# Kernel tuning notes

Hardware: AMD Instinct MI355X
Metric: run time of the kernel (lower is better)

## Reference

```python
import jax, jax.numpy as jnp
import numpy as np

EMB = 256
N_NODES = 100000
N_EDGES = 500000
N_REL = 10
REL_DIM = 64
HID = 128
HEADS = 4
HEAD_DIM = HID // HEADS


def setup_inputs() -> dict:
    key = jax.random.key(0)
    ks = jax.random.split(key, 16)
    s = lambda i, shape: jax.random.normal(ks[i], shape, dtype=jnp.float32) * 0.05
    return {
        "node_embeddings": jax.random.normal(ks[0], (N_NODES, EMB), dtype=jnp.float32),
        "edge_index": jax.random.randint(ks[1], (2, N_EDGES), 0, N_NODES),
        "relation_type": jax.random.randint(ks[2], (N_EDGES,), 0, N_REL),
        "rel_emb": s(3, (N_REL, REL_DIM)),
        "W_edge": s(4, (2 * EMB, HID)), "b_edge": jnp.zeros((HID,), jnp.float32),
        "W_q": s(5, (REL_DIM, HID)), "b_q": jnp.zeros((HID,), jnp.float32),
        "W_k": s(6, (HID, HID)), "b_k": jnp.zeros((HID,), jnp.float32),
        "W_v": s(7, (HID, HID)), "b_v": jnp.zeros((HID,), jnp.float32),
        "W_o1": s(8, (HID, HID)), "b_o1": jnp.zeros((HID,), jnp.float32),
        "W_o2": s(9, (HID, 1)), "b_o2": jnp.zeros((1,), jnp.float32),
    }


def reference(node_embeddings, edge_index, relation_type, rel_emb,
              W_edge, b_edge, W_q, b_q, W_k, b_k, W_v, b_v,
              W_o1, b_o1, W_o2, b_o2):
    # Gather endpoint features: [E, 2*EMB]
    src = node_embeddings[edge_index[0]]
    tgt = node_embeddings[edge_index[1]]
    edge_features = jnp.concatenate([src, tgt], axis=1)
    # Edge MLP (dropout is identity at eval): [E, HID]
    edge_hidden = jax.nn.relu(edge_features @ W_edge + b_edge)
    # Relation embedding lookup: [E, REL_DIM]
    rel = rel_emb[relation_type]
    E = edge_hidden.shape[0]
    Q = (rel @ W_q + b_q).reshape(E, HEADS, HEAD_DIM)
    K = (edge_hidden @ W_k + b_k).reshape(E, HEADS, HEAD_DIM)
    V = (edge_hidden @ W_v + b_v).reshape(E, HEADS, HEAD_DIM)
    scale = jnp.sqrt(jnp.float32(HEAD_DIM))
    scores = jnp.sum(Q * K, axis=-1) / scale          # [E, HEADS]
    attn = jax.nn.softmax(scores, axis=-1)            # softmax over heads
    attended = (attn[..., None] * V).reshape(E, HID)
    output = attended + edge_hidden
    # Output MLP: Linear->ReLU->Linear(1)
    h = jax.nn.relu(output @ W_o1 + b_o1)
    score = (h @ W_o2 + b_o2).squeeze(-1)             # [E]
    return score
```

## Files before the change

### kernel.cpp

```cpp
#include <hip/hip_runtime.h>

#define EMB   256
#define HID   128
#define RELD  64
#define NREL  10
#define TE    128

typedef __attribute__((ext_vector_type(8)))  short bf16x8;
typedef __attribute__((ext_vector_type(16))) float f32x16;

__device__ __forceinline__ float bf16_to_f32(unsigned short u) {
    union { unsigned int i; float f; } v;
    v.i = ((unsigned int)u) << 16;
    return v.f;
}

__device__ __forceinline__ unsigned short f32_to_bf16(float x) {
    union { unsigned int i; float f; } v;
    v.f = x;
    unsigned int b = v.i;
    unsigned int rounded = b + 0x7fffu + ((b >> 16) & 1u);
    return (unsigned short)(rounded >> 16);
}

template <bool F32>
__device__ __forceinline__ float ldx(const void* p, size_t i) {
    if (F32) return ((const float*)p)[i];
    return bf16_to_f32(((const unsigned short*)p)[i]);
}

__device__ __forceinline__ bool detect_f32(const void* nodeEmb) {
    const float* f = (const float*)nodeEmb;
    float x = f[(threadIdx.x & 63) * 997];
    bool sane = isfinite(x) && fabsf(x) < 1.0e6f;
    unsigned long long m = __ballot(sane);
    return __popcll(m) >= 48;
}

__device__ __forceinline__ void gload16(const void* g, void* l) {
    __builtin_amdgcn_global_load_lds(
        (const __attribute__((address_space(1))) unsigned int*)g,
        (__attribute__((address_space(3))) unsigned int*)l, 16, 0, 0);
}

#define WAITVL(n) asm volatile("s_waitcnt vmcnt(" #n ") lgkmcnt(0)" ::: "memory")

__device__ __forceinline__ void sbar() {
    __builtin_amdgcn_sched_barrier(0);
    __builtin_amdgcn_s_barrier();
    __builtin_amdgcn_sched_barrier(0);
}
__device__ __forceinline__ void bar_lds() {
    asm volatile("s_waitcnt lgkmcnt(0)" ::: "memory");
    sbar();
}

template <bool F32>
__device__ void prep_body(int vb, const void* W_edge, const void* W_k,
                          const void* W_v, const void* W_o1, const void* rel_emb,
                          const void* W_q, const void* b_q,
                          unsigned short* WTe, unsigned short* WTk,
                          unsigned short* WTv, unsigned short* WTo1, float* Qtab)
{
    if (vb < 448) {
        int idx = vb * 256 + threadIdx.x;
        if (idx < 65536) {
            int kc = idx >> 12, e = idx & 4095;
            int g = e >> 3, j = e & 7;
            int col = g & 127, kg = g >> 7;
            int k = kc * 32 + kg * 8 + j;
            WTe[idx] = f32_to_bf16(ldx<F32>(W_edge, (size_t)k * HID + col));
        } else if (idx < 65536 + 16384) {
            int i = idx - 65536;
            int kc = i >> 12, e = i & 4095;
            int g = e >> 3, j = e & 7;
            int col = g & 127, kg = (g >> 7) & 3;
            int k = kc * 32 + kg * 8 + j;
            WTk[i] = f32_to_bf16(ldx<F32>(W_k, (size_t)k * HID + col));
        } else if (idx < 65536 + 2 * 16384) {
            int i = idx - 65536 - 16384;
            int kc = i >> 12, e = i & 4095;
            int g = e >> 3, j = e & 7;
            int col = g & 127, kg = (g >> 7) & 3;
            int k = kc * 32 + kg * 8 + j;
            WTv[i] = f32_to_bf16(ldx<F32>(W_v, (size_t)k * HID + col));
        } else {
            int i = idx - 65536 - 2 * 16384;
            int kc = i >> 12, e = i & 4095;
            int g = e >> 3, j = e & 7;
            int col = g & 127, kg = (g >> 7) & 3;
            int k = kc * 32 + kg * 8 + j;
            WTo1[i] = f32_to_bf16(ldx<F32>(W_o1, (size_t)k * HID + col));
        }
    } else {
        const int t = threadIdx.x;
        const int c = t & (HID - 1);
        const int h = t >> 7;
        for (int r = h; r < NREL; r += 2) {
            float acc = 0.f;
            for (int d = 0; d < RELD; ++d)
                acc += ldx<F32>(rel_emb, r * RELD + d) * ldx<F32>(W_q, (size_t)d * HID + c);
            Qtab[r * HID + c] = acc + ldx<F32>(b_q, c);
        }
    }
}

__global__ void prep_kernel(const void* nodeEmb,
                            const void* W_edge, const void* W_k, const void* W_v,
                            const void* W_o1, const void* rel_emb, const void* W_q,
                            const void* b_q,
                            unsigned short* WTe, unsigned short* WTk,
                            unsigned short* WTv, unsigned short* WTo1, float* Qtab,
                            unsigned short* nodeBf16, int convBlocks,
                            unsigned long long nodeElems)
{
    bool f32 = detect_f32(nodeEmb);
    int b = blockIdx.x;
    if (b < convBlocks) {
        if (!f32) return;
        unsigned long long i = (unsigned long long)b * 2048ull + threadIdx.x * 8;
        if (i + 8 <= nodeElems) {
            const float* src = (const float*)nodeEmb + i;
            float4 f0 = *(const float4*)src;
            float4 f1 = *(const float4*)(src + 4);
            union { unsigned short us[8]; uint4 v; } pk;
            pk.us[0] = f32_to_bf16(f0.x); pk.us[1] = f32_to_bf16(f0.y);
            pk.us[2] = f32_to_bf16(f0.z); pk.us[3] = f32_to_bf16(f0.w);
            pk.us[4] = f32_to_bf16(f1.x); pk.us[5] = f32_to_bf16(f1.y);
            pk.us[6] = f32_to_bf16(f1.z); pk.us[7] = f32_to_bf16(f1.w);
            *(uint4*)(nodeBf16 + i) = pk.v;
        }
        return;
    }
    b -= convBlocks;
    if (f32) prep_body<true >(b, W_edge, W_k, W_v, W_o1, rel_emb, W_q, b_q,
                              WTe, WTk, WTv, WTo1, Qtab);
    else     prep_body<false>(b, W_edge, W_k, W_v, W_o1, rel_emb, W_q, b_q,
                              WTe, WTk, WTv, WTo1, Qtab);
}

struct __align__(16) Smem {
    unsigned short sHid[16 * 128 * 8];
    unsigned short SA[2][4096];
    unsigned short SB[2][4096];
    float sQf[NREL * HID];
    float sBias[5 * HID];
    float sSc[TE][4];
    float sAttn[TE][4];
    float sPart[TE][2];
    int   sSrc[TE], sTgt[TE], sRel[TE];
};

__device__ __forceinline__ int shid_idx(int row, int k) {
    return (((k >> 3) * 128 + row) << 3) + (k & 7);
}

template <bool F32, bool GBF16>
__device__ void fused_body(
    Smem& sm,
    const void* gsrc, const int* edgeIdx, const int* relType,
    const unsigned short* WTe, const unsigned short* WTk,
    const unsigned short* WTv, const unsigned short* WTo1,
    const void* b_edge, const void* b_k, const void* b_v,
    const void* b_o1, const void* W_o2, const void* b_o2,
    const float* Qtab, void* outp, int E)
{
    const int t   = threadIdx.x;
    const int l   = t & 63;
    const int w   = t >> 6;
    const int c   = l & 31;
    const int h5  = l >> 5;
    const int rt  = w >> 1;
    const int cg2 = w & 1;
    const int bs  = blockIdx.x * TE;
    const int aRow = 32 * rt + c;

    if (t < TE) {
        int e = bs + t;
        if (e >= E) e = E - 1;
        if (e < 0)  e = 0;
        sm.sSrc[t] = edgeIdx[e];
        sm.sTgt[t] = edgeIdx[E + e];
        int r = relType[e];
        if (r < 0) r = 0;
        if (r >= NREL) r = NREL - 1;
        sm.sRel[t] = r;
    }
    for (int i = t; i < 5 * HID; i += 512) {
        int which = i >> 7, j = i & (HID - 1);
        float v = (which == 0) ? ldx<F32>(b_edge, j)
                : (which == 1) ? ldx<F32>(b_k, j)
                : (which == 2) ? ldx<F32>(b_v, j)
                : (which == 3) ? ldx<F32>(b_o1, j)
                               : ldx<F32>(W_o2, j);
        sm.sBias[i] = v;
    }
    for (int i = t; i < NREL * HID; i += 512)
        sm.sQf[i] = Qtab[i];
    __syncthreads();

    const int    stRow = t & 127;
    const size_t rowOffS = (size_t)sm.sSrc[stRow] * EMB;
    const size_t rowOffT = (size_t)sm.sTgt[stRow] * EMB;
    const int    colSub  = (t >> 8) * 16 + ((t >> 7) & 1) * 8;
    char* const  ldsWaveA0 = (char*)sm.SA[0] + w * 1024;
    char* const  ldsWaveA1 = (char*)sm.SA[1] + w * 1024;
    char* const  ldsWaveB0 = (char*)sm.SB[0] + w * 1024;
    char* const  ldsWaveB1 = (char*)sm.SB[1] + w * 1024;

    #define STAGE_A(kc, buf)                                                     \
    {                                                                            \
        size_t eoff = (((kc) < 8) ? rowOffS : rowOffT)                           \
                      + (size_t)(((kc) & 7) * 32 + colSub);                      \
        if (GBF16) {                                                             \
            gload16((const unsigned short*)gsrc + eoff,                          \
                    (buf) ? ldsWaveA1 : ldsWaveA0);                              \
        } else {                                                                 \
            const float* p_ = (const float*)gsrc + eoff;                         \
            float4 f0_ = *(const float4*)p_;                                     \
            float4 f1_ = *(const float4*)(p_ + 4);                               \
            union { unsigned short us[8]; uint4 v; } pk_;                        \
            pk_.us[0] = f32_to_bf16(f0_.x); pk_.us[1] = f32_to_bf16(f0_.y);      \
            pk_.us[2] = f32_to_bf16(f0_.z); pk_.us[3] = f32_to_bf16(f0_.w);      \
            pk_.us[4] = f32_to_bf16(f1_.x); pk_.us[5] = f32_to_bf16(f1_.y);      \
            pk_.us[6] = f32_to_bf16(f1_.z); pk_.us[7] = f32_to_bf16(f1_.w);      \
            *(uint4*)((char*)sm.SA[(buf)] + t * 16) = pk_.v;                     \
        }                                                                        \
    }

    #define STAGE_B(WT, kc, buf)                                                 \
        gload16((WT) + (kc) * 4096 + t * 8, (buf) ? ldsWaveB1 : ldsWaveB0);

    #define MFMA_SA(buf, accv)                                                   \
    {                                                                            \
        const char* sa_ = (const char*)sm.SA[(buf)];                             \
        const char* sb_ = (const char*)sm.SB[(buf)];                             \
        _Pragma("unroll")                                                        \
        for (int s_ = 0; s_ < 2; ++s_) {                                         \
            bf16x8 a_ = *(const bf16x8*)(sa_ + ((s_ * 256 + h5 * 128 + aRow) << 4)); \
            _Pragma("unroll")                                                    \
            for (int ct_ = 0; ct_ < 2; ++ct_) {                                  \
                bf16x8 b_ = *(const bf16x8*)                                     \
                    (sb_ + ((s_ * 256 + h5 * 128 + 64 * cg2 + 32 * ct_ + c) << 4)); \
                accv[ct_] = __builtin_amdgcn_mfma_f32_32x32x16_bf16(             \
                                a_, b_, accv[ct_], 0, 0, 0);                     \
            }                                                                    \
        }                                                                        \
    }

    #define MFMA_H(kc, buf, accv)                                                \
    {                                                                            \
        const char* sb_ = (const char*)sm.SB[(buf)];                             \
        _Pragma("unroll")                                                        \
        for (int s_ = 0; s_ < 2; ++s_) {                                         \
            bf16x8 a_ = *(const bf16x8*)((const char*)sm.sHid +                  \
                         ((((kc) * 4 + s_ * 2 + h5) * 128 + aRow) << 4));        \
            _Pragma("unroll")                                                    \
            for (int ct_ = 0; ct_ < 2; ++ct_) {                                  \
                bf16x8 b_ = *(const bf16x8*)                                     \
                    (sb_ + ((s_ * 256 + h5 * 128 + 64 * cg2 + 32 * ct_ + c) << 4)); \
                accv[ct_] = __builtin_amdgcn_mfma_f32_32x32x16_bf16(             \
                                a_, b_, accv[ct_], 0, 0, 0);                     \
            }                                                                    \
        }                                                                        \
    }

    f32x16 acc[2];
    acc[0] = (f32x16)(0.0f); acc[1] = (f32x16)(0.0f);
    STAGE_A(0, 0); STAGE_B(WTe, 0, 0);
    STAGE_A(1, 1); STAGE_B(WTe, 1, 1);
    #pragma unroll
    for (int kc = 0; kc < 16; ++kc) {
        int buf = kc & 1;
        if (kc < 15) { WAITVL(2); } else { WAITVL(0); }
        sbar();
        MFMA_SA(buf, acc);
        sbar();
        if (kc < 14) { STAGE_A(kc + 2, buf); STAGE_B(WTe, kc + 2, buf); }
    }
    STAGE_B(WTk, 0, 0); STAGE_B(WTk, 1, 1);
    {
        #pragma unroll
        for (int ct = 0; ct < 2; ++ct) {
            int col = 64 * cg2 + 32 * ct + c;
            float bb = sm.sBias[col];
            #pragma unroll
            for (int r = 0; r < 16; ++r) {
                int erow = 32 * rt + (r & 3) + 8 * (r >> 2) + 4 * h5;
                sm.sHid[shid_idx(erow, col)] = f32_to_bf16(fmaxf(acc[ct][r] + bb, 0.f));
            }
        }
    }
    bar_lds();

    f32x16 kacc[2];
    kacc[0] = (f32x16)(0.0f); kacc[1] = (f32x16)(0.0f);
    #pragma unroll
    for (int kc = 0; kc < 4; ++kc) {
        int buf = kc & 1;
        if (kc < 3) { WAITVL(1); } else { WAITVL(0); }
        sbar();
        MFMA_H(kc, buf, kacc);
        sbar();
        if (kc < 2) STAGE_B(WTk, kc + 2, buf);
    }
    STAGE_B(WTv, 0, 0); STAGE_B(WTv, 1, 1);

    {
        float ps[2][16];
        #pragma unroll
        for (int ct = 0; ct < 2; ++ct) {
            int col = 64 * cg2 + 32 * ct + c;
            float bk = sm.sBias[HID + col];
            #pragma unroll
            for (int r = 0; r < 16; ++r) {
                int erow = 32 * rt + (r & 3) + 8 * (r >> 2) + 4 * h5;
                ps[ct][r] = (kacc[ct][r] + bk) * sm.sQf[sm.sRel[erow] * HID + col];
            }
        }
        #pragma unroll
        for (int m = 1; m < 32; m <<= 1)
            #pragma unroll
            for (int ct = 0; ct < 2; ++ct)
                #pragma unroll
                for (int r = 0; r < 16; ++r)
                    ps[ct][r] += __shfl_xor(ps[ct][r], m, 64);
        if (c == 0) {
            const float inv = 0.17677669529663687f;
            #pragma unroll
            for (int ct = 0; ct < 2; ++ct) {
                int head = 2 * cg2 + ct;
                #pragma unroll
                for (int r = 0; r < 16; ++r) {
                    int erow = 32 * rt + (r & 3) + 8 * (r >> 2) + 4 * h5;
                    sm.sSc[erow][head] = ps[ct][r] * inv;
                }
            }
        }
    }
    bar_lds();
    if (t < TE) {
        float s0 = sm.sSc[t][0], s1 = sm.sSc[t][1];
        float s2 = sm.sSc[t][2], s3 = sm.sSc[t][3];
        float m = fmaxf(fmaxf(s0, s1), fmaxf(s2, s3));
        float e0 = expf(s0 - m), e1 = expf(s1 - m);
        float e2 = expf(s2 - m), e3 = expf(s3 - m);
        float den = e0 + e1 + e2 + e3;
        sm.sAttn[t][0] = e0 / den; sm.sAttn[t][1] = e1 / den;
        sm.sAttn[t][2] = e2 / den; sm.sAttn[t][3] = e3 / den;
    }
    bar_lds();

    f32x16 vacc[2];
    vacc[0] = (f32x16)(0.0f); vacc[1] = (f32x16)(0.0f);
    #pragma unroll
    for (int kc = 0; kc < 4; ++kc) {
        int buf = kc & 1;
        if (kc < 3) { WAITVL(1); } else { WAITVL(0); }
        sbar();
        MFMA_H(kc, buf, vacc);
        sbar();
        if (kc < 2) STAGE_B(WTv, kc + 2, buf);
    }
    STAGE_B(WTo1, 0, 0); STAGE_B(WTo1, 1, 1);

    {
        #pragma unroll
        for (int ct = 0; ct < 2; ++ct) {
            int col  = 64 * cg2 + 32 * ct + c;
            int head = 2 * cg2 + ct;
            float bv = sm.sBias[2 * HID + col];
            #pragma unroll
            for (int r = 0; r < 16; ++r) {
                int erow = 32 * rt + (r & 3) + 8 * (r >> 2) + 4 * h5;
                float at = sm.sAttn[erow][head];
                int   si = shid_idx(erow, col);
                float hv = bf16_to_f32(sm.sHid[si]);
                sm.sHid[si] = f32_to_bf16(at * (vacc[ct][r] + bv) + hv);
            }
        }
    }
    bar_lds();

    f32x16 oacc[2];
    oacc[0] = (f32x16)(0.0f); oacc[1] = (f32x16)(0.0f);
    #pragma unroll
    for (int kc = 0; kc < 4; ++kc) {
        int buf = kc & 1;
        if (kc < 3) { WAITVL(1); } else { WAITVL(0); }
        sbar();
        MFMA_H(kc, buf, oacc);
        sbar();
        if (kc < 2) STAGE_B(WTo1, kc + 2, buf);
    }
    {
        float pr[16];
        #pragma unroll
        for (int r = 0; r < 16; ++r) pr[r] = 0.f;
        #pragma unroll
        for (int ct = 0; ct < 2; ++ct) {
            int col = 64 * cg2 + 32 * ct + c;
            float bo = sm.sBias[3 * HID + col];
            float wo = sm.sBias[4 * HID + col];
            #pragma unroll
            for (int r = 0; r < 16; ++r)
                pr[r] += fmaxf(oacc[ct][r] + bo, 0.f) * wo;
        }
        #pragma unroll
        for (int m = 1; m < 32; m <<= 1)
            #pragma unroll
            for (int r = 0; r < 16; ++r)
                pr[r] += __shfl_xor(pr[r], m, 64);
        if (c == 0) {
            #pragma unroll
            for (int r = 0; r < 16; ++r) {
                int erow = 32 * rt + (r & 3) + 8 * (r >> 2) + 4 * h5;
                sm.sPart[erow][cg2] = pr[r];
            }
        }
    }
    bar_lds();
    if (t < TE) {
        int ge = bs + t;
        if (ge < E) {
            float val = sm.sPart[t][0] + sm.sPart[t][1] + ldx<F32>(b_o2, 0);
            if (F32) ((float*)outp)[ge] = val;
            else     ((unsigned short*)outp)[ge] = f32_to_bf16(val);
        }
    }

    #undef STAGE_A
    #undef STAGE_B
    #undef MFMA_SA
    #undef MFMA_H
}

__global__ __launch_bounds__(512, 4) void RelationAttentionMLPHead_10539849744626_kernel(
    const void* nodeEmb, const unsigned short* nodeBf16, int useConv,
    const int* edgeIdx, const int* relType,
    const unsigned short* WTe, const unsigned short* WTk,
    const unsigned short* WTv, const unsigned short* WTo1,
    const void* b_edge, const void* b_k, const void* b_v,
    const void* b_o1, const void* W_o2, const void* b_o2,
    const float* Qtab, void* outp, int E)
{
    __shared__ Smem sm;
    if (detect_f32(nodeEmb)) {
        if (useConv)
            fused_body<true, true >(sm, nodeBf16, edgeIdx, relType, WTe, WTk, WTv, WTo1,
                                    b_edge, b_k, b_v, b_o1, W_o2, b_o2, Qtab, outp, E);
        else
            fused_body<true, false>(sm, nodeEmb, edgeIdx, relType, WTe, WTk, WTv, WTo1,
                                    b_edge, b_k, b_v, b_o1, W_o2, b_o2, Qtab, outp, E);
    } else {
        fused_body<false, true>(sm, nodeEmb, edgeIdx, relType, WTe, WTk, WTv, WTo1,
                                b_edge, b_k, b_v, b_o1, W_o2, b_o2, Qtab, outp, E);
    }
}

extern "C" void kernel_launch(void* const* d_in, const int* in_sizes, int n_in,
                              void* d_out, int out_size, void* d_ws, size_t ws_size,
                              hipStream_t stream) {
    (void)n_in;

    const void* nodeEmb = d_in[0];
    const int*  edgeIdx = (const int*)d_in[1];
    const int*  relType = (const int*)d_in[2];
    const void* rel_emb = d_in[3];
    const void* W_edge  = d_in[4];
    const void* b_edge  = d_in[5];
    const void* W_q     = d_in[6];
    const void* b_q     = d_in[7];
    const void* W_k     = d_in[8];
    const void* b_k     = d_in[9];
    const void* W_v     = d_in[10];
    const void* b_v     = d_in[11];
    const void* W_o1    = d_in[12];
    const void* b_o1    = d_in[13];
    const void* W_o2    = d_in[14];
    const void* b_o2    = d_in[15];

    int E = out_size;
    if (E <= 0) E = in_sizes ? in_sizes[2] : 0;
    if (E <= 0) E = 500000;

    unsigned long long nodeElems =
        (in_sizes && in_sizes[0] > 0) ? (unsigned long long)in_sizes[0] : 25600000ull;

    char* ws = (char*)d_ws;
    float*          Qtab     = (float*)ws;
    unsigned short* WTe      = (unsigned short*)(ws + 8192);
    unsigned short* WTk      = (unsigned short*)(ws + 139264);
    unsigned short* WTv      = (unsigned short*)(ws + 172032);
    unsigned short* WTo1     = (unsigned short*)(ws + 204800);
    unsigned short* nodeBf16 = (unsigned short*)(ws + 237568);

    size_t need = 237568ull + nodeElems * 2ull;
    int useConv = (ws_size >= need) ? 1 : 0;
    int convBlocks = useConv ? (int)((nodeElems + 2047ull) / 2048ull) : 0;

    prep_kernel<<<convBlocks + 449, 256, 0, stream>>>(
        nodeEmb, W_edge, W_k, W_v, W_o1, rel_emb, W_q, b_q,
        WTe, WTk, WTv, WTo1, Qtab, nodeBf16, convBlocks, nodeElems);

    int grid = (E + TE - 1) / TE;
    if (grid < 1) grid = 1;

    RelationAttentionMLPHead_10539849744626_kernel<<<grid, 512, 0, stream>>>(
        nodeEmb, nodeBf16, useConv, edgeIdx, relType, WTe, WTk, WTv, WTo1,
        b_edge, b_k, b_v, b_o1, W_o2, b_o2, Qtab, d_out, E);
}
```

Before: 435.0 us.

## Load gathered A operands directly into registers with 3-deep prefetch, pad hidden LDS

The first GEMM's gathered node rows are no longer staged through LDS. Each lane loads its MFMA A fragment straight from global memory into registers, using a 4-slot ring that prefetches three k-chunks ahead, while B tiles still go through LDS. The LDS A buffers are removed and the hidden-activation LDS stride is padded from 128 to 130 rows, intended to reduce bank conflicts. This adds VGPR pressure and relies on hand-tuned vmcnt wait counts, which must match the mixed register and LDS loads to stay correct.

Measured after the change: 428.3 us. Within noise of the previous version (-1.5%).

```diff
diff --git a/kernel.cpp b/kernel.cpp
--- a/kernel.cpp
+++ b/kernel.cpp
@@ -5,6 +5,7 @@
 #define RELD  64
 #define NREL  10
 #define TE    128
+#define SHSTR 130
 
 typedef __attribute__((ext_vector_type(8)))  short bf16x8;
 typedef __attribute__((ext_vector_type(16))) float f32x16;
@@ -140,8 +141,7 @@
 }
 
 struct __align__(16) Smem {
-    unsigned short sHid[16 * 128 * 8];
-    unsigned short SA[2][4096];
+    unsigned short sHid[16 * SHSTR * 8];
     unsigned short SB[2][4096];
     float sQf[NREL * HID];
     float sBias[5 * HID];
@@ -152,7 +152,24 @@
 };
 
 __device__ __forceinline__ int shid_idx(int row, int k) {
-    return (((k >> 3) * 128 + row) << 3) + (k & 7);
+    return (((k >> 3) * SHSTR + row) << 3) + (k & 7);
+}
+
+template <bool GBF16>
+__device__ __forceinline__ bf16x8 loadA8(const void* row, int off) {
+    if (GBF16) {
+        return *(const bf16x8*)((const unsigned short*)row + off);
+    } else {
+        const float* p = (const float*)row + off;
+        float4 f0 = *(const float4*)p;
+        float4 f1 = *(const float4*)(p + 4);
+        union { unsigned short us[8]; bf16x8 v; } pk;
+        pk.us[0] = f32_to_bf16(f0.x); pk.us[1] = f32_to_bf16(f0.y);
+        pk.us[2] = f32_to_bf16(f0.z); pk.us[3] = f32_to_bf16(f0.w);
+        pk.us[4] = f32_to_bf16(f1.x); pk.us[5] = f32_to_bf16(f1.y);
+        pk.us[6] = f32_to_bf16(f1.z); pk.us[7] = f32_to_bf16(f1.w);
+        return pk.v;
+    }
 }
 
 template <bool F32, bool GBF16>
@@ -199,45 +216,46 @@
         sm.sQf[i] = Qtab[i];
     __syncthreads();
 
-    const int    stRow = t & 127;
-    const size_t rowOffS = (size_t)sm.sSrc[stRow] * EMB;
-    const size_t rowOffT = (size_t)sm.sTgt[stRow] * EMB;
-    const int    colSub  = (t >> 8) * 16 + ((t >> 7) & 1) * 8;
-    char* const  ldsWaveA0 = (char*)sm.SA[0] + w * 1024;
-    char* const  ldsWaveA1 = (char*)sm.SA[1] + w * 1024;
-    char* const  ldsWaveB0 = (char*)sm.SB[0] + w * 1024;
-    char* const  ldsWaveB1 = (char*)sm.SB[1] + w * 1024;
-
-    #define STAGE_A(kc, buf)                                                     \
-    {                                                                            \
-        size_t eoff = (((kc) < 8) ? rowOffS : rowOffT)                           \
-                      + (size_t)(((kc) & 7) * 32 + colSub);                      \
-        if (GBF16) {                                                             \
-            gload16((const unsigned short*)gsrc + eoff,                          \
-                    (buf) ? ldsWaveA1 : ldsWaveA0);                              \
-        } else {                                                                 \
-            const float* p_ = (const float*)gsrc + eoff;                         \
-            float4 f0_ = *(const float4*)p_;                                     \
-            float4 f1_ = *(const float4*)(p_ + 4);                               \
-            union { unsigned short us[8]; uint4 v; } pk_;                        \
-            pk_.us[0] = f32_to_bf16(f0_.x); pk_.us[1] = f32_to_bf16(f0_.y);      \
-            pk_.us[2] = f32_to_bf16(f0_.z); pk_.us[3] = f32_to_bf16(f0_.w);      \
-            pk_.us[4] = f32_to_bf16(f1_.x); pk_.us[5] = f32_to_bf16(f1_.y);      \
-            pk_.us[6] = f32_to_bf16(f1_.z); pk_.us[7] = f32_to_bf16(f1_.w);      \
-            *(uint4*)((char*)sm.SA[(buf)] + t * 16) = pk_.v;                     \
-        }                                                                        \
-    }
-
+    const void* rowSrc;
+    const void* rowTgt;
+    if (GBF16) {
+        rowSrc = (const void*)((const unsigned short*)gsrc + (size_t)sm.sSrc[aRow] * EMB);
+        rowTgt = (const void*)((const unsigned short*)gsrc + (size_t)sm.sTgt[aRow] * EMB);
+    } else {
+        rowSrc = (const void*)((const float*)gsrc + (size_t)sm.sSrc[aRow] * EMB);
+        rowTgt = (const void*)((const float*)gsrc + (size_t)sm.sTgt[aRow] * EMB);
+    }
+
+    char* const ldsWaveB0 = (char*)sm.SB[0] + w * 1024;
+    char* const ldsWaveB1 = (char*)sm.SB[1] + w * 1024;
+
+    #define LOAD_A(kc, s) \
+        loadA8<GBF16>(((kc) < 8) ? rowSrc : rowTgt, ((kc) & 7) * 32 + (s) * 16 + h5 * 8)
     #define STAGE_B(WT, kc, buf)                                                 \
         gload16((WT) + (kc) * 4096 + t * 8, (buf) ? ldsWaveB1 : ldsWaveB0);
 
-    #define MFMA_SA(buf, accv)                                                   \
+    #define MFMA_AR(slot, buf, accv)                                             \
     {                                                                            \
-        const char* sa_ = (const char*)sm.SA[(buf)];                             \
         const char* sb_ = (const char*)sm.SB[(buf)];                             \
         _Pragma("unroll")                                                        \
         for (int s_ = 0; s_ < 2; ++s_) {                                         \
-            bf16x8 a_ = *(const bf16x8*)(sa_ + ((s_ * 256 + h5 * 128 + aRow) << 4)); \
+            _Pragma("unroll")                                                    \
+            for (int ct_ = 0; ct_ < 2; ++ct_) {                                  \
+                bf16x8 b_ = *(const bf16x8*)                                     \
+                    (sb_ + ((s_ * 256 + h5 * 128 + 64 * cg2 + 32 * ct_ + c) << 4)); \
+                accv[ct_] = __builtin_amdgcn_mfma_f32_32x32x16_bf16(             \
+                                aR[slot][s_], b_, accv[ct_], 0, 0, 0);           \
+            }                                                                    \
+        }                                                                        \
+    }
+
+    #define MFMA_H(kc, buf, accv)                                                \
+    {                                                                            \
+        const char* sb_ = (const char*)sm.SB[(buf)];                             \
+        _Pragma("unroll")                                                        \
+        for (int s_ = 0; s_ < 2; ++s_) {                                         \
+            bf16x8 a_ = *(const bf16x8*)((const char*)sm.sHid +                  \
+                         ((((kc) * 4 + s_ * 2 + h5) * SHSTR + aRow) << 4));      \
             _Pragma("unroll")                                                    \
             for (int ct_ = 0; ct_ < 2; ++ct_) {                                  \
                 bf16x8 b_ = *(const bf16x8*)                                     \
@@ -248,35 +266,33 @@
         }                                                                        \
     }
 
-    #define MFMA_H(kc, buf, accv)                                                \
-    {                                                                            \
-        const char* sb_ = (const char*)sm.SB[(buf)];                             \
-        _Pragma("unroll")                                                        \
-        for (int s_ = 0; s_ < 2; ++s_) {                                         \
-            bf16x8 a_ = *(const bf16x8*)((const char*)sm.sHid +                  \
-                         ((((kc) * 4 + s_ * 2 + h5) * 128 + aRow) << 4));        \
-            _Pragma("unroll")                                                    \
-            for (int ct_ = 0; ct_ < 2; ++ct_) {                                  \
-                bf16x8 b_ = *(const bf16x8*)                                     \
-                    (sb_ + ((s_ * 256 + h5 * 128 + 64 * cg2 + 32 * ct_ + c) << 4)); \
-                accv[ct_] = __builtin_amdgcn_mfma_f32_32x32x16_bf16(             \
-                                a_, b_, accv[ct_], 0, 0, 0);                     \
-            }                                                                    \
-        }                                                                        \
-    }
-
     f32x16 acc[2];
     acc[0] = (f32x16)(0.0f); acc[1] = (f32x16)(0.0f);
-    STAGE_A(0, 0); STAGE_B(WTe, 0, 0);
-    STAGE_A(1, 1); STAGE_B(WTe, 1, 1);
-    #pragma unroll
-    for (int kc = 0; kc < 16; ++kc) {
-        int buf = kc & 1;
-        if (kc < 15) { WAITVL(2); } else { WAITVL(0); }
-        sbar();
-        MFMA_SA(buf, acc);
-        sbar();
-        if (kc < 14) { STAGE_A(kc + 2, buf); STAGE_B(WTe, kc + 2, buf); }
+    {
+        bf16x8 aR[4][2];
+        #pragma unroll
+        for (int p = 0; p < 3; ++p) {
+            aR[p][0] = LOAD_A(p, 0);
+            aR[p][1] = LOAD_A(p, 1);
+        }
+        STAGE_B(WTe, 0, 0);
+        STAGE_B(WTe, 1, 1);
+        #pragma unroll
+        for (int kc = 0; kc < 16; ++kc) {
+            int buf = kc & 1;
+            if (kc == 0)      { WAITVL(1); }
+            else if (kc < 14) { WAITVL(3); }
+            else if (kc == 14){ WAITVL(1); }
+            else              { WAITVL(0); }
+            sbar();
+            MFMA_AR((kc & 3), buf, acc);
+            sbar();
+            if (kc < 13) {
+                aR[(kc + 3) & 3][0] = LOAD_A(kc + 3, 0);
+                aR[(kc + 3) & 3][1] = LOAD_A(kc + 3, 1);
+            }
+            if (kc < 14) STAGE_B(WTe, kc + 2, buf);
+        }
     }
     STAGE_B(WTk, 0, 0); STAGE_B(WTk, 1, 1);
     {
@@ -429,9 +445,9 @@
         }
     }
 
-    #undef STAGE_A
+    #undef LOAD_A
     #undef STAGE_B
-    #undef MFMA_SA
+    #undef MFMA_AR
     #undef MFMA_H
 }
 
```
